# Performance work log

Measured on AMD Instinct MI355X. Metric: run time of the kernel, lower is better.

Reference implementation:

```python
import jax, jax.numpy as jnp
import numpy as np

EPS = 1e-5

def conv3x3(x, W, b):
    # NCHW 3x3 conv, padding=1 (SAME)
    y = jax.lax.conv_general_dilated(x, W, (1, 1), ((1, 1), (1, 1)),
                                     dimension_numbers=('NCHW', 'OIHW', 'NCHW'))
    return y + b[None, :, None, None]

def bn_relu(x, gamma, beta):
    # BatchNorm2d in training mode: batch statistics over (N,H,W)
    m = x.mean(axis=(0, 2, 3), keepdims=True)
    v = x.var(axis=(0, 2, 3), keepdims=True)
    xn = (x - m) * jax.lax.rsqrt(v + EPS)
    return jax.nn.relu(xn * gamma[None, :, None, None] + beta[None, :, None, None])

def haar_dwt2(x):
    # pywt.dwt2(x, 'db1') for even H,W: cA=LL, cH=row-detail/col-approx,
    # cV=row-approx/col-detail, cD=HH; each 0.5*(+-a +-b +-c +-d)
    a = x[:, :, 0::2, 0::2]
    b = x[:, :, 0::2, 1::2]
    c = x[:, :, 1::2, 0::2]
    d = x[:, :, 1::2, 1::2]
    cA = (a + b + c + d) * 0.5
    cH = (a + b - c - d) * 0.5
    cV = (a - b + c - d) * 0.5
    cD = (a - b - c + d) * 0.5
    return jnp.concatenate([cA, cH, cV, cD], axis=1)  # [B, 4C, H/2, W/2]

def setup_inputs() -> dict:
    key = jax.random.key(0)
    ks = jax.random.split(key, 4)
    B, Cin, Cout, H, W = 8, 64, 128, 256, 256
    inputs = jax.random.normal(ks[0], (B, Cin, H, W), dtype=jnp.float32)
    W1 = jax.random.normal(ks[1], (Cout, Cin, 3, 3), dtype=jnp.float32) * 0.05
    W2 = jax.random.normal(ks[2], (Cout, Cout, 3, 3), dtype=jnp.float32) * 0.05
    W3 = jax.random.normal(ks[3], (Cout, 4 * Cout, 3, 3), dtype=jnp.float32) * 0.05
    z = jnp.zeros((Cout,), jnp.float32)
    o = jnp.ones((Cout,), jnp.float32)
    return {"inputs": inputs,
            "W1": W1, "b1": z, "g1": o, "be1": z,
            "W2": W2, "b2": z, "g2": o, "be2": z,
            "W3": W3, "b3": z, "g3": o, "be3": z}

def reference(inputs, W1, b1, g1, be1, W2, b2, g2, be2, W3, b3, g3, be3):
    h = bn_relu(conv3x3(inputs, W1, b1), g1, be1)
    skip_con = bn_relu(conv3x3(h, W2, b2), g2, be2)          # [B, out_c, H, W]
    # original detaches before the pywt round-trip
    dwt = haar_dwt2(jax.lax.stop_gradient(skip_con))          # [B, 4*out_c, H/2, W/2]
    dwt_out = bn_relu(conv3x3(dwt, W3, b3), g3, be3)          # [B, out_c, H/2, W/2]
    return (skip_con, dwt_out)
```

## Files before the change

### kernel.cpp

```cpp
#include <hip/hip_runtime.h>

typedef __attribute__((ext_vector_type(8))) short bf16x8;
typedef __attribute__((ext_vector_type(4))) short bf16x4;
typedef __attribute__((ext_vector_type(4))) float f32x4;

__device__ __forceinline__ float bf2f(ushort u) {
  union { unsigned int i; float f; } v; v.i = ((unsigned int)u) << 16; return v.f;
}
__device__ __forceinline__ ushort f2bf(float f) {
  union { float f; unsigned int i; } v; v.f = f;
  unsigned int x = v.i;
  unsigned int r = (x + 0x7fffu + ((x >> 16) & 1u)) >> 16;
  return (ushort)r;
}

__device__ __forceinline__ void gload_lds16(const ushort* g, ushort* l) {
  __builtin_amdgcn_global_load_lds((const __attribute__((address_space(1))) void*)g,
                                   (__attribute__((address_space(3))) void*)l, 16, 0, 0);
}

__global__ void zero_f32(float* p, int n) {
  int i = blockIdx.x * 256 + threadIdx.x;
  if (i < n) p[i] = 0.f;
}

__global__ void pack_w(const float* __restrict__ W, ushort* __restrict__ Wp, int Cin) {
  int ncic = Cin >> 5;
  int total = 9 * ncic * 8 * 64 * 8;
  for (int idx = blockIdx.x * 256 + threadIdx.x; idx < total; idx += gridDim.x * 256) {
    int j = idx & 7;
    int l = (idx >> 3) & 63;
    int cf = (idx >> 9) & 7;
    int rest = idx >> 12;
    int cic = rest % ncic;
    int tap = rest / ncic;
    int co = cf * 16 + (l & 15);
    int ci = cic * 32 + ((l >> 4) * 8) + j;
    int ky = tap / 3, kx = tap % 3;
    Wp[idx] = f2bf(W[((co * Cin + ci) * 3 + ky) * 3 + kx]);
  }
}

__global__ __launch_bounds__(256)
void nchw2nhwc(const float* __restrict__ in, ushort* __restrict__ out) {
  const int n  = blockIdx.y;
  const int p0 = blockIdx.x << 6;
  const int tid = threadIdx.x;
  __shared__ ushort t[64 * 72];
  {
    int c  = tid >> 2;
    int pq = (tid & 3) << 4;
    const float* ip = in + (((size_t)(n * 64 + c)) << 16) + p0 + pq;
#pragma unroll
    for (int k = 0; k < 4; ++k) {
      float4 f = *(const float4*)(ip + k * 4);
      int p = pq + k * 4;
      t[(p + 0) * 72 + c] = f2bf(f.x);
      t[(p + 1) * 72 + c] = f2bf(f.y);
      t[(p + 2) * 72 + c] = f2bf(f.z);
      t[(p + 3) * 72 + c] = f2bf(f.w);
    }
  }
  __syncthreads();
#pragma unroll
  for (int k = 0; k < 2; ++k) {
    int id = k * 256 + tid;
    int cj = id & 7, p = id >> 3;
    bf16x8 v = *(const bf16x8*)&t[p * 72 + cj * 8];
    *(bf16x8*)(out + ((((size_t)n << 16) + p0 + p) << 6) + cj * 8) = v;
  }
}

__device__ __forceinline__ bf16x8 bnrelu8(bf16x8 v, const float* __restrict__ coef, int c0) {
  float4 a0 = *(const float4*)(coef + c0);
  float4 a1 = *(const float4*)(coef + c0 + 4);
  float4 b0 = *(const float4*)(coef + 128 + c0);
  float4 b1 = *(const float4*)(coef + 128 + c0 + 4);
  bf16x8 r;
  r[0] = (short)f2bf(fmaxf(a0.x * bf2f((ushort)v[0]) + b0.x, 0.f));
  r[1] = (short)f2bf(fmaxf(a0.y * bf2f((ushort)v[1]) + b0.y, 0.f));
  r[2] = (short)f2bf(fmaxf(a0.z * bf2f((ushort)v[2]) + b0.z, 0.f));
  r[3] = (short)f2bf(fmaxf(a0.w * bf2f((ushort)v[3]) + b0.w, 0.f));
  r[4] = (short)f2bf(fmaxf(a1.x * bf2f((ushort)v[4]) + b1.x, 0.f));
  r[5] = (short)f2bf(fmaxf(a1.y * bf2f((ushort)v[5]) + b1.y, 0.f));
  r[6] = (short)f2bf(fmaxf(a1.z * bf2f((ushort)v[6]) + b1.z, 0.f));
  r[7] = (short)f2bf(fmaxf(a1.w * bf2f((ushort)v[7]) + b1.w, 0.f));
  return r;
}

template<int MODE>
__global__ __launch_bounds__(256)
void conv_reg(const ushort* __restrict__ src, const ushort* __restrict__ Wp,
              const float* __restrict__ bias, const float* __restrict__ coef,
              ushort* __restrict__ out, float* __restrict__ sSum, float* __restrict__ sSsq,
              int Cin, int H, int W)
{
  const int ncic = Cin >> 5;
  const int x0 = blockIdx.x << 6;
  const int y0 = blockIdx.y << 1;
  const int n  = blockIdx.z;
  const int tid = threadIdx.x;
  const int wv = tid >> 6, l = tid & 63, l15 = l & 15, l4 = l >> 4;

  __shared__ __align__(16) char smem[17408];
  ushort* lds = (ushort*)smem;
  ushort* eps = (ushort*)smem;

  f32x4 acc[2][2][4];
#pragma unroll
  for (int yr = 0; yr < 2; ++yr)
#pragma unroll
    for (int f = 0; f < 2; ++f)
#pragma unroll
      for (int xf = 0; xf < 4; ++xf) acc[yr][f][xf] = (f32x4){0.f, 0.f, 0.f, 0.f};

  const size_t HW = (size_t)H * W;

  for (int cic = 0; cic < ncic; ++cic) {
    __syncthreads();
    for (int i = tid; i < 1056; i += 256) {
      int cj = i & 3;
      int t = i >> 2;
      int row = t / 66;
      int xt = t - row * 66;
      int ry = y0 + row - 1;
      int gx = x0 + xt - 1;
      bf16x8 v = {};
      if ((unsigned)ry < (unsigned)H && (unsigned)gx < (unsigned)W) {
        const ushort* p = src + ((size_t)n * HW + (size_t)ry * W + gx) * Cin + (cic << 5) + (cj << 3);
        v = *(const bf16x8*)p;
        if (MODE == 1) v = bnrelu8(v, coef, (cic << 5) + (cj << 3));
      }
      *(bf16x8*)&lds[(((row << 2) | cj) * 66 + xt) << 3] = v;
    }
    __syncthreads();

#pragma unroll
    for (int tap = 0; tap < 9; ++tap) {
      const int ky = tap / 3, kx = tap % 3;
      bf16x8 afr[2];
#pragma unroll
      for (int f = 0; f < 2; ++f) {
        const int cf = (wv << 1) | f;
        afr[f] = *(const bf16x8*)(Wp + (((size_t)(tap * ncic + cic) * 8 + cf) * 64 + l) * 8);
      }
      bf16x8 bfr[2][4];
#pragma unroll
      for (int yr = 0; yr < 2; ++yr)
#pragma unroll
        for (int xf = 0; xf < 4; ++xf) {
          int row = yr + ky;
          int xt = (xf << 4) + l15 + kx;
          bfr[yr][xf] = *(const bf16x8*)&lds[(((row << 2) | l4) * 66 + xt) << 3];
        }
#pragma unroll
      for (int f = 0; f < 2; ++f)
#pragma unroll
        for (int yr = 0; yr < 2; ++yr)
#pragma unroll
          for (int xf = 0; xf < 4; ++xf)
            acc[yr][f][xf] = __builtin_amdgcn_mfma_f32_16x16x32_bf16(afr[f], bfr[yr][xf], acc[yr][f][xf], 0, 0, 0);
    }
  }

  float sm[2][4] = {{0.f}}, sq[2][4] = {{0.f}};
  const int cb = (wv << 5) + (l4 << 2);
  for (int yr = 0; yr < 2; ++yr) {
    __syncthreads();
#pragma unroll
    for (int f = 0; f < 2; ++f) {
      const int cf = cb + (f << 4);
      float4 bv = *(const float4*)(bias + cf);
#pragma unroll
      for (int xf = 0; xf < 4; ++xf) {
        float v0 = acc[yr][f][xf][0] + bv.x;
        float v1 = acc[yr][f][xf][1] + bv.y;
        float v2 = acc[yr][f][xf][2] + bv.z;
        float v3 = acc[yr][f][xf][3] + bv.w;
        sm[f][0] += v0; sq[f][0] += v0 * v0;
        sm[f][1] += v1; sq[f][1] += v1 * v1;
        sm[f][2] += v2; sq[f][2] += v2 * v2;
        sm[f][3] += v3; sq[f][3] += v3 * v3;
        bf16x4 u;
        u[0] = (short)f2bf(v0); u[1] = (short)f2bf(v1);
        u[2] = (short)f2bf(v2); u[3] = (short)f2bf(v3);
        *(bf16x4*)&eps[((xf << 4) + l15) * 136 + cf] = u;
      }
    }
    __syncthreads();
    {
      const int xx = tid >> 2, c0 = (tid & 3) << 5;
      ushort* op = out + ((size_t)n * HW + (size_t)(y0 + yr) * W + x0 + xx) * 128 + c0;
#pragma unroll
      for (int k = 0; k < 4; ++k)
        *(bf16x8*)(op + (k << 3)) = *(const bf16x8*)&eps[xx * 136 + c0 + (k << 3)];
    }
  }

  const int rep = (int)((blockIdx.z * gridDim.y + blockIdx.y) * gridDim.x + blockIdx.x) & 31;
#pragma unroll
  for (int f = 0; f < 2; ++f)
#pragma unroll
    for (int j = 0; j < 4; ++j) {
      float s = sm[f][j], q = sq[f][j];
#pragma unroll
      for (int o = 1; o < 16; o <<= 1) { s += __shfl_xor(s, o); q += __shfl_xor(q, o); }
      if (l15 == 0) {
        int co = cb + (f << 4) + j;
        atomicAdd(&sSum[rep * 128 + co], s);
        atomicAdd(&sSsq[rep * 128 + co], q);
      }
    }
}

__global__ __launch_bounds__(256)
void conv_dma(const ushort* __restrict__ src, const ushort* __restrict__ Wp,
              const float* __restrict__ bias,
              ushort* __restrict__ out, float* __restrict__ sSum, float* __restrict__ sSsq,
              int Cin, int H, int W)
{
  const int ncic = Cin >> 5;
  const int x0 = blockIdx.x << 6;
  const int y0 = blockIdx.y << 1;
  const int n  = blockIdx.z;
  const int tid = threadIdx.x;
  const int wv = tid >> 6, l = tid & 63, l15 = l & 15, l4 = l >> 4;

  __shared__ __align__(16) ushort smem[2 * 8448];

  const size_t HW = (size_t)H * W;
  const ushort* srcn = src + (size_t)n * HW * Cin;

  int off[5];
#pragma unroll
  for (int it = 0; it < 5; ++it) {
    int i = it * 256 + tid;
    int cj = i & 3, p = i >> 2;
    int row = p / 66, xt = p - row * 66;
    int ry = y0 + row - 1, gx = x0 + xt - 1;
    bool ok = (i < 1056) && ((unsigned)ry < (unsigned)H) && ((unsigned)gx < (unsigned)W);
    off[it] = ok ? (int)((ry * W + gx) * Cin + (cj << 3)) : -1;
  }

  if (x0 == 0 || x0 + 64 >= W || y0 == 0 || y0 + 2 >= H) {
    for (int k = tid; k < 2112; k += 256) *(bf16x8*)&smem[k << 3] = (bf16x8){};
  }
  __syncthreads();

  f32x4 acc[2][2][4];
#pragma unroll
  for (int yr = 0; yr < 2; ++yr)
#pragma unroll
    for (int f = 0; f < 2; ++f)
#pragma unroll
      for (int xf = 0; xf < 4; ++xf) acc[yr][f][xf] = (f32x4){0.f, 0.f, 0.f, 0.f};

  auto STAGE = [&](ushort* buf, int cic) {
    const int coff = cic << 5;
#pragma unroll
    for (int it = 0; it < 5; ++it) {
      ushort* ldst = buf + ((it < 4 ? (it * 256 + (wv << 6)) : 1024) << 3);
      if (off[it] >= 0)
        gload_lds16(srcn + off[it] + coff, ldst);
    }
  };

  auto COMPUTE = [&](const ushort* buf, int cic) {
#pragma unroll
    for (int tap = 0; tap < 9; ++tap) {
      const int ky = tap / 3, kx = tap % 3;
      bf16x8 afr[2];
#pragma unroll
      for (int f = 0; f < 2; ++f) {
        const int cf = (wv << 1) | f;
        afr[f] = *(const bf16x8*)(Wp + (((size_t)(tap * ncic + cic) * 8 + cf) * 64 + l) * 8);
      }
      bf16x8 bfr[2][4];
#pragma unroll
      for (int yr = 0; yr < 2; ++yr)
#pragma unroll
        for (int xf = 0; xf < 4; ++xf) {
          int row = yr + ky;
          int xt = (xf << 4) + l15 + kx;
          bfr[yr][xf] = *(const bf16x8*)&buf[((((row * 66 + xt) << 2) | l4)) << 3];
        }
#pragma unroll
      for (int f = 0; f < 2; ++f)
#pragma unroll
        for (int yr = 0; yr < 2; ++yr)
#pragma unroll
          for (int xf = 0; xf < 4; ++xf)
            acc[yr][f][xf] = __builtin_amdgcn_mfma_f32_16x16x32_bf16(afr[f], bfr[yr][xf], acc[yr][f][xf], 0, 0, 0);
    }
  };

  STAGE(smem, 0);
  __syncthreads();

  int cur = 0;
  for (int cic = 0; cic < ncic; ++cic) {
    if (cic + 1 < ncic) STAGE(smem + (cur ^ 1) * 8448, cic + 1);
    COMPUTE(smem + cur * 8448, cic);
    __syncthreads();
    cur ^= 1;
  }

  float sm[2][4] = {{0.f}}, sq[2][4] = {{0.f}};
  ushort* eps = smem;
  const int cb = (wv << 5) + (l4 << 2);
  for (int yr = 0; yr < 2; ++yr) {
    __syncthreads();
#pragma unroll
    for (int f = 0; f < 2; ++f) {
      const int cf = cb + (f << 4);
      float4 bv = *(const float4*)(bias + cf);
#pragma unroll
      for (int xf = 0; xf < 4; ++xf) {
        float v0 = acc[yr][f][xf][0] + bv.x;
        float v1 = acc[yr][f][xf][1] + bv.y;
        float v2 = acc[yr][f][xf][2] + bv.z;
        float v3 = acc[yr][f][xf][3] + bv.w;
        sm[f][0] += v0; sq[f][0] += v0 * v0;
        sm[f][1] += v1; sq[f][1] += v1 * v1;
        sm[f][2] += v2; sq[f][2] += v2 * v2;
        sm[f][3] += v3; sq[f][3] += v3 * v3;
        bf16x4 u;
        u[0] = (short)f2bf(v0); u[1] = (short)f2bf(v1);
        u[2] = (short)f2bf(v2); u[3] = (short)f2bf(v3);
        *(bf16x4*)&eps[((xf << 4) + l15) * 136 + cf] = u;
      }
    }
    __syncthreads();
    {
      const int xx = tid >> 2, c0 = (tid & 3) << 5;
      ushort* op = out + ((size_t)n * HW + (size_t)(y0 + yr) * W + x0 + xx) * 128 + c0;
#pragma unroll
      for (int k = 0; k < 4; ++k)
        *(bf16x8*)(op + (k << 3)) = *(const bf16x8*)&eps[xx * 136 + c0 + (k << 3)];
    }
  }

  const int rep = (int)((blockIdx.z * gridDim.y + blockIdx.y) * gridDim.x + blockIdx.x) & 31;
#pragma unroll
  for (int f = 0; f < 2; ++f)
#pragma unroll
    for (int j = 0; j < 4; ++j) {
      float s = sm[f][j], q = sq[f][j];
#pragma unroll
      for (int o = 1; o < 16; o <<= 1) { s += __shfl_xor(s, o); q += __shfl_xor(q, o); }
      if (l15 == 0) {
        int co = cb + (f << 4) + j;
        atomicAdd(&sSum[rep * 128 + co], s);
        atomicAdd(&sSsq[rep * 128 + co], q);
      }
    }
}

__global__ void bn_finalize(const float* __restrict__ sSum, const float* __restrict__ sSsq,
                            const float* __restrict__ g, const float* __restrict__ be,
                            float* __restrict__ coef, float invN)
{
  int c = threadIdx.x;
  float S = 0.f, Q = 0.f;
  for (int r = 0; r < 32; ++r) { S += sSum[r * 128 + c]; Q += sSsq[r * 128 + c]; }
  float m = S * invN;
  float v = Q * invN - m * m;
  float a = g[c] / sqrtf(v + 1e-5f);
  coef[c] = a;
  coef[128 + c] = be[c] - m * a;
}

__global__ __launch_bounds__(256)
void skip_dwt2(const ushort* __restrict__ skipRaw, const float* __restrict__ coef,
               float* __restrict__ outSkip, ushort* __restrict__ dwt)
{
  const int x0 = blockIdx.x << 6;
  const int oy = blockIdx.y;
  const int n  = blockIdx.z >> 2;
  const int ct = blockIdx.z & 3;
  const int y0 = oy << 1;
  const int tid = threadIdx.x;
  __shared__ float t32[32 * 2 * 68];

#pragma unroll
  for (int it = 0; it < 2; ++it) {
    int i = it * 256 + tid;
    int cj = i & 3, x = (i >> 2) & 63, r = i >> 8;
    int c0 = (ct << 5) + (cj << 3);
    bf16x8 v = *(const bf16x8*)(skipRaw + (((size_t)n << 16) + (size_t)(y0 + r) * 256 + x0 + x) * 128 + c0);
    float4 a0 = *(const float4*)(coef + c0);
    float4 a1 = *(const float4*)(coef + c0 + 4);
    float4 b0 = *(const float4*)(coef + 128 + c0);
    float4 b1 = *(const float4*)(coef + 128 + c0 + 4);
    float av[8] = {a0.x, a0.y, a0.z, a0.w, a1.x, a1.y, a1.z, a1.w};
    float bv[8] = {b0.x, b0.y, b0.z, b0.w, b1.x, b1.y, b1.z, b1.w};
    int cl = cj << 3;
#pragma unroll
    for (int k = 0; k < 8; ++k)
      t32[((cl + k) * 2 + r) * 68 + x] = fmaxf(av[k] * bf2f((ushort)v[k]) + bv[k], 0.f);
  }
  __syncthreads();

  {
    int c = tid >> 3, x8 = (tid & 7) << 3;
    float* op = outSkip + (((size_t)(n * 128 + (ct << 5) + c)) << 16) + (size_t)y0 * 256 + x0 + x8;
#pragma unroll
    for (int r = 0; r < 2; ++r) {
      float4 r0 = *(const float4*)&t32[(c * 2 + r) * 68 + x8];
      float4 r1 = *(const float4*)&t32[(c * 2 + r) * 68 + x8 + 4];
      *(float4*)(op + (size_t)r * 256) = r0;
      *(float4*)(op + (size_t)r * 256 + 4) = r1;
    }
  }

  if (tid < 128) {
    int cj = tid & 3, ox = tid >> 2;
    int cl = cj << 3;
    bf16x8 oA, oH, oV, oD;
#pragma unroll
    for (int k = 0; k < 8; ++k) {
      int c = cl + k;
      float p00 = t32[(c * 2 + 0) * 68 + 2 * ox];
      float p01 = t32[(c * 2 + 0) * 68 + 2 * ox + 1];
      float p10 = t32[(c * 2 + 1) * 68 + 2 * ox];
      float p11 = t32[(c * 2 + 1) * 68 + 2 * ox + 1];
      oA[k] = (short)f2bf((p00 + p01 + p10 + p11) * 0.5f);
      oH[k] = (short)f2bf((p00 + p01 - p10 - p11) * 0.5f);
      oV[k] = (short)f2bf((p00 - p01 + p10 - p11) * 0.5f);
      oD[k] = (short)f2bf((p00 - p01 - p10 + p11) * 0.5f);
    }
    size_t db = ((size_t)n * 16384 + (size_t)oy * 128 + (x0 >> 1) + ox) * 512 + (ct << 5) + cl;
    *(bf16x8*)(dwt + db)       = oA;
    *(bf16x8*)(dwt + db + 128) = oH;
    *(bf16x8*)(dwt + db + 256) = oV;
    *(bf16x8*)(dwt + db + 384) = oD;
  }
}

__global__ __launch_bounds__(256)
void bn_transpose_out(const ushort* __restrict__ src, const float* __restrict__ coef,
                      float* __restrict__ dst, int H, int W)
{
  const int n  = blockIdx.z >> 2;
  const int cc = blockIdx.z & 3;
  const int x0 = blockIdx.x << 6;
  const int y  = blockIdx.y;
  const int tid = threadIdx.x;
  __shared__ float t[32 * 68];
  const size_t HW = (size_t)H * W;
  {
    int p = tid >> 2, cj = tid & 3;
    int c0 = (cc << 5) + (cj << 3);
    bf16x8 v = *(const bf16x8*)(src + ((size_t)n * HW + (size_t)y * W + x0 + p) * 128 + c0);
    float4 a0 = *(const float4*)(coef + c0);
    float4 a1 = *(const float4*)(coef + c0 + 4);
    float4 b0 = *(const float4*)(coef + 128 + c0);
    float4 b1 = *(const float4*)(coef + 128 + c0 + 4);
    int cl = cj << 3;
    t[(cl + 0) * 68 + p] = fmaxf(a0.x * bf2f((ushort)v[0]) + b0.x, 0.f);
    t[(cl + 1) * 68 + p] = fmaxf(a0.y * bf2f((ushort)v[1]) + b0.y, 0.f);
    t[(cl + 2) * 68 + p] = fmaxf(a0.z * bf2f((ushort)v[2]) + b0.z, 0.f);
    t[(cl + 3) * 68 + p] = fmaxf(a0.w * bf2f((ushort)v[3]) + b0.w, 0.f);
    t[(cl + 4) * 68 + p] = fmaxf(a1.x * bf2f((ushort)v[4]) + b1.x, 0.f);
    t[(cl + 5) * 68 + p] = fmaxf(a1.y * bf2f((ushort)v[5]) + b1.y, 0.f);
    t[(cl + 6) * 68 + p] = fmaxf(a1.z * bf2f((ushort)v[6]) + b1.z, 0.f);
    t[(cl + 7) * 68 + p] = fmaxf(a1.w * bf2f((ushort)v[7]) + b1.w, 0.f);
  }
  __syncthreads();
  {
    int c = tid >> 3, x8 = (tid & 7) << 3;
    float4 r0 = *(const float4*)&t[c * 68 + x8];
    float4 r1 = *(const float4*)&t[c * 68 + x8 + 4];
    float* op = dst + ((size_t)(n * 128 + (cc << 5) + c)) * HW + (size_t)y * W + x0 + x8;
    *(float4*)op = r0;
    *(float4*)(op + 4) = r1;
  }
}

extern "C" void kernel_launch(void* const* d_in, const int* in_sizes, int n_in,
                              void* d_out, int out_size, void* d_ws, size_t ws_size,
                              hipStream_t stream)
{
  const float* input = (const float*)d_in[0];
  const float* W1  = (const float*)d_in[1];
  const float* b1  = (const float*)d_in[2];
  const float* g1  = (const float*)d_in[3];
  const float* be1 = (const float*)d_in[4];
  const float* W2  = (const float*)d_in[5];
  const float* b2  = (const float*)d_in[6];
  const float* g2  = (const float*)d_in[7];
  const float* be2 = (const float*)d_in[8];
  const float* W3  = (const float*)d_in[9];
  const float* b3  = (const float*)d_in[10];
  const float* g3  = (const float*)d_in[11];
  const float* be3 = (const float*)d_in[12];

  char* ws = (char*)d_ws;
  ushort* h_raw    = (ushort*)(ws + 0);
  ushort* skip_raw = (ushort*)(ws + 134217728);
  ushort* dwt      = (ushort*)(ws + 268435456);
  ushort* in_nhwc  = (ushort*)(ws + 268435456);
  ushort* raw3     = (ushort*)(ws + 402653184);
  float*  stats    = (float*)(ws + 436207616);
  float*  s1 = stats,          *q1 = stats + 4096;
  float*  s2 = stats + 8192,   *q2 = stats + 12288;
  float*  s3 = stats + 16384,  *q3 = stats + 20480;
  float*  coef = (float*)(ws + 436305920);
  float*  c1 = coef, *c2 = coef + 256, *c3 = coef + 512;
  ushort* Wp1 = (ushort*)(ws + 436308992);
  ushort* Wp2 = (ushort*)(ws + 436456448);
  ushort* Wp3 = (ushort*)(ws + 436751360);

  zero_f32<<<96, 256, 0, stream>>>(stats, 24576);
  pack_w<<<288, 256, 0, stream>>>(W1, Wp1, 64);
  pack_w<<<576, 256, 0, stream>>>(W2, Wp2, 128);
  pack_w<<<2304, 256, 0, stream>>>(W3, Wp3, 512);
  nchw2nhwc<<<dim3(1024, 8), 256, 0, stream>>>(input, in_nhwc);

  conv_dma<<<dim3(4, 128, 8), 256, 0, stream>>>(in_nhwc, Wp1, b1,
                                                h_raw, s1, q1, 64, 256, 256);
  bn_finalize<<<1, 128, 0, stream>>>(s1, q1, g1, be1, c1, 1.f / 524288.f);

  conv_reg<1><<<dim3(4, 128, 8), 256, 0, stream>>>(h_raw, Wp2, b2, c1,
                                                   skip_raw, s2, q2, 128, 256, 256);
  bn_finalize<<<1, 128, 0, stream>>>(s2, q2, g2, be2, c2, 1.f / 524288.f);

  skip_dwt2<<<dim3(4, 128, 32), 256, 0, stream>>>(skip_raw, c2, (float*)d_out, dwt);

  conv_dma<<<dim3(2, 64, 8), 256, 0, stream>>>(dwt, Wp3, b3,
                                               raw3, s3, q3, 512, 128, 128);
  bn_finalize<<<1, 128, 0, stream>>>(s3, q3, g3, be3, c3, 1.f / 131072.f);

  bn_transpose_out<<<dim3(2, 128, 32), 256, 0, stream>>>(raw3, c3, (float*)d_out + 67108864, 128, 128);
}
```

Before: 696.3 us.

## Sweep conv down 16 rows with rolling 4-row LDS ring buffer

Replaces the per-2-row conv_reg kernel with conv_yp. Each block now walks 16 output rows and keeps a 4-row circular buffer of all input channels in LDS, so halo rows are loaded once instead of being reloaded by neighbouring blocks. It is also used for conv1 in place of conv_dma. The grid shrinks 8x, which costs parallelism and adds serial stage/compute phases with no overlap between the loads and the MFMA work. The LDS footprint grows to about 72KB, which lowers occupancy.

Measured after the change: 755.8 us. +8.6%, slower.

```diff
diff --git a/kernel.cpp b/kernel.cpp
--- a/kernel.cpp
+++ b/kernel.cpp
@@ -88,116 +88,135 @@
   return r;
 }
 
-template<int MODE>
+template<int MODE, int NCIC>
 __global__ __launch_bounds__(256)
-void conv_reg(const ushort* __restrict__ src, const ushort* __restrict__ Wp,
-              const float* __restrict__ bias, const float* __restrict__ coef,
-              ushort* __restrict__ out, float* __restrict__ sSum, float* __restrict__ sSsq,
-              int Cin, int H, int W)
+void conv_yp(const ushort* __restrict__ src, const ushort* __restrict__ Wp,
+             const float* __restrict__ bias, const float* __restrict__ coef,
+             ushort* __restrict__ out, float* __restrict__ sSum, float* __restrict__ sSsq,
+             int H, int W)
 {
-  const int ncic = Cin >> 5;
+  constexpr int Cin = NCIC * 32;
+  constexpr int CIP = 136;
+  constexpr int PLANE = 66 * CIP;
   const int x0 = blockIdx.x << 6;
-  const int y0 = blockIdx.y << 1;
+  const int ysBase = blockIdx.y << 4;
   const int n  = blockIdx.z;
   const int tid = threadIdx.x;
   const int wv = tid >> 6, l = tid & 63, l15 = l & 15, l4 = l >> 4;
 
-  __shared__ __align__(16) char smem[17408];
-  ushort* lds = (ushort*)smem;
-  ushort* eps = (ushort*)smem;
-
-  f32x4 acc[2][2][4];
-#pragma unroll
-  for (int yr = 0; yr < 2; ++yr)
-#pragma unroll
-    for (int f = 0; f < 2; ++f)
-#pragma unroll
-      for (int xf = 0; xf < 4; ++xf) acc[yr][f][xf] = (f32x4){0.f, 0.f, 0.f, 0.f};
+  __shared__ __align__(16) ushort smem[4 * PLANE];
 
   const size_t HW = (size_t)H * W;
-
-  for (int cic = 0; cic < ncic; ++cic) {
-    __syncthreads();
-    for (int i = tid; i < 1056; i += 256) {
-      int cj = i & 3;
-      int t = i >> 2;
-      int row = t / 66;
-      int xt = t - row * 66;
-      int ry = y0 + row - 1;
+  const ushort* srcn = src + (size_t)n * HW * Cin;
+
+  auto STAGE2 = [&](int r0) {
+    constexpr int NCJ = NCIC * 4;
+    constexpr int NCH = 2 * 66 * NCJ;
+    for (int i = tid; i < NCH; i += 256) {
+      int cj = i & (NCJ - 1);
+      int t  = i / NCJ;
+      int xt = t % 66;
+      int r  = t / 66;
+      int ry = r0 + r;
       int gx = x0 + xt - 1;
       bf16x8 v = {};
       if ((unsigned)ry < (unsigned)H && (unsigned)gx < (unsigned)W) {
-        const ushort* p = src + ((size_t)n * HW + (size_t)ry * W + gx) * Cin + (cic << 5) + (cj << 3);
-        v = *(const bf16x8*)p;
-        if (MODE == 1) v = bnrelu8(v, coef, (cic << 5) + (cj << 3));
-      }
-      *(bf16x8*)&lds[(((row << 2) | cj) * 66 + xt) << 3] = v;
-    }
-    __syncthreads();
-
-#pragma unroll
-    for (int tap = 0; tap < 9; ++tap) {
-      const int ky = tap / 3, kx = tap % 3;
-      bf16x8 afr[2];
-#pragma unroll
-      for (int f = 0; f < 2; ++f) {
-        const int cf = (wv << 1) | f;
-        afr[f] = *(const bf16x8*)(Wp + (((size_t)(tap * ncic + cic) * 8 + cf) * 64 + l) * 8);
-      }
-      bf16x8 bfr[2][4];
-#pragma unroll
-      for (int yr = 0; yr < 2; ++yr)
-#pragma unroll
-        for (int xf = 0; xf < 4; ++xf) {
-          int row = yr + ky;
-          int xt = (xf << 4) + l15 + kx;
-          bfr[yr][xf] = *(const bf16x8*)&lds[(((row << 2) | l4) * 66 + xt) << 3];
-        }
-#pragma unroll
-      for (int f = 0; f < 2; ++f)
-#pragma unroll
-        for (int yr = 0; yr < 2; ++yr)
-#pragma unroll
-          for (int xf = 0; xf < 4; ++xf)
-            acc[yr][f][xf] = __builtin_amdgcn_mfma_f32_16x16x32_bf16(afr[f], bfr[yr][xf], acc[yr][f][xf], 0, 0, 0);
-    }
-  }
+        v = *(const bf16x8*)(srcn + ((size_t)ry * W + gx) * Cin + (cj << 3));
+        if (MODE == 1) v = bnrelu8(v, coef, cj << 3);
+      }
+      *(bf16x8*)&smem[(ry & 3) * PLANE + xt * CIP + (cj << 3)] = v;
+    }
+  };
+
+  STAGE2(ysBase - 1);
+  STAGE2(ysBase + 1);
+  __syncthreads();
 
   float sm[2][4] = {{0.f}}, sq[2][4] = {{0.f}};
   const int cb = (wv << 5) + (l4 << 2);
-  for (int yr = 0; yr < 2; ++yr) {
+  const int rep = (int)((blockIdx.z * gridDim.y + blockIdx.y) * gridDim.x + blockIdx.x) & 31;
+
+  for (int step = 0; step < 8; ++step) {
+    const int ys = ysBase + (step << 1);
+
+    f32x4 acc[2][2][4];
+#pragma unroll
+    for (int yr = 0; yr < 2; ++yr)
+#pragma unroll
+      for (int f = 0; f < 2; ++f)
+#pragma unroll
+        for (int xf = 0; xf < 4; ++xf) acc[yr][f][xf] = (f32x4){0.f, 0.f, 0.f, 0.f};
+
+    for (int cic = 0; cic < NCIC; ++cic) {
+#pragma unroll
+      for (int tap = 0; tap < 9; ++tap) {
+        const int ky = tap / 3, kx = tap % 3;
+        bf16x8 afr[2];
+#pragma unroll
+        for (int f = 0; f < 2; ++f) {
+          const int cf = (wv << 1) | f;
+          afr[f] = *(const bf16x8*)(Wp + (((size_t)(tap * NCIC + cic) * 8 + cf) * 64 + l) * 8);
+        }
+        bf16x8 bfr[2][4];
+#pragma unroll
+        for (int yr = 0; yr < 2; ++yr)
+#pragma unroll
+          for (int xf = 0; xf < 4; ++xf) {
+            int aRow = ys + yr - 1 + ky;
+            bfr[yr][xf] = *(const bf16x8*)&smem[(aRow & 3) * PLANE +
+                                               ((xf << 4) + l15 + kx) * CIP +
+                                               (cic << 5) + (l4 << 3)];
+          }
+#pragma unroll
+        for (int f = 0; f < 2; ++f)
+#pragma unroll
+          for (int yr = 0; yr < 2; ++yr)
+#pragma unroll
+            for (int xf = 0; xf < 4; ++xf)
+              acc[yr][f][xf] = __builtin_amdgcn_mfma_f32_16x16x32_bf16(afr[f], bfr[yr][xf], acc[yr][f][xf], 0, 0, 0);
+      }
+    }
+
     __syncthreads();
-#pragma unroll
-    for (int f = 0; f < 2; ++f) {
-      const int cf = cb + (f << 4);
-      float4 bv = *(const float4*)(bias + cf);
-#pragma unroll
-      for (int xf = 0; xf < 4; ++xf) {
-        float v0 = acc[yr][f][xf][0] + bv.x;
-        float v1 = acc[yr][f][xf][1] + bv.y;
-        float v2 = acc[yr][f][xf][2] + bv.z;
-        float v3 = acc[yr][f][xf][3] + bv.w;
-        sm[f][0] += v0; sq[f][0] += v0 * v0;
-        sm[f][1] += v1; sq[f][1] += v1 * v1;
-        sm[f][2] += v2; sq[f][2] += v2 * v2;
-        sm[f][3] += v3; sq[f][3] += v3 * v3;
-        bf16x4 u;
-        u[0] = (short)f2bf(v0); u[1] = (short)f2bf(v1);
-        u[2] = (short)f2bf(v2); u[3] = (short)f2bf(v3);
-        *(bf16x4*)&eps[((xf << 4) + l15) * 136 + cf] = u;
+    ushort* eps = &smem[((ys - 1) & 3) * PLANE];
+    for (int yr = 0; yr < 2; ++yr) {
+      if (yr) __syncthreads();
+#pragma unroll
+      for (int f = 0; f < 2; ++f) {
+        const int cf = cb + (f << 4);
+        float4 bv = *(const float4*)(bias + cf);
+#pragma unroll
+        for (int xf = 0; xf < 4; ++xf) {
+          float v0 = acc[yr][f][xf][0] + bv.x;
+          float v1 = acc[yr][f][xf][1] + bv.y;
+          float v2 = acc[yr][f][xf][2] + bv.z;
+          float v3 = acc[yr][f][xf][3] + bv.w;
+          sm[f][0] += v0; sq[f][0] += v0 * v0;
+          sm[f][1] += v1; sq[f][1] += v1 * v1;
+          sm[f][2] += v2; sq[f][2] += v2 * v2;
+          sm[f][3] += v3; sq[f][3] += v3 * v3;
+          bf16x4 u;
+          u[0] = (short)f2bf(v0); u[1] = (short)f2bf(v1);
+          u[2] = (short)f2bf(v2); u[3] = (short)f2bf(v3);
+          *(bf16x4*)&eps[((xf << 4) + l15) * 136 + cf] = u;
+        }
+      }
+      __syncthreads();
+      {
+        const int xx = tid >> 2, c0 = (tid & 3) << 5;
+        ushort* op = out + ((size_t)n * HW + (size_t)(ys + yr) * W + x0 + xx) * 128 + c0;
+#pragma unroll
+        for (int k = 0; k < 4; ++k)
+          *(bf16x8*)(op + (k << 3)) = *(const bf16x8*)&eps[xx * 136 + c0 + (k << 3)];
       }
     }
     __syncthreads();
-    {
-      const int xx = tid >> 2, c0 = (tid & 3) << 5;
-      ushort* op = out + ((size_t)n * HW + (size_t)(y0 + yr) * W + x0 + xx) * 128 + c0;
-#pragma unroll
-      for (int k = 0; k < 4; ++k)
-        *(bf16x8*)(op + (k << 3)) = *(const bf16x8*)&eps[xx * 136 + c0 + (k << 3)];
-    }
-  }
-
-  const int rep = (int)((blockIdx.z * gridDim.y + blockIdx.y) * gridDim.x + blockIdx.x) & 31;
+    if (step < 7) {
+      STAGE2(ys + 3);
+      __syncthreads();
+    }
+  }
+
 #pragma unroll
   for (int f = 0; f < 2; ++f)
 #pragma unroll
@@ -517,12 +536,12 @@
   pack_w<<<2304, 256, 0, stream>>>(W3, Wp3, 512);
   nchw2nhwc<<<dim3(1024, 8), 256, 0, stream>>>(input, in_nhwc);
 
-  conv_dma<<<dim3(4, 128, 8), 256, 0, stream>>>(in_nhwc, Wp1, b1,
-                                                h_raw, s1, q1, 64, 256, 256);
+  conv_yp<0, 2><<<dim3(4, 16, 8), 256, 0, stream>>>(in_nhwc, Wp1, b1, nullptr,
+                                                    h_raw, s1, q1, 256, 256);
   bn_finalize<<<1, 128, 0, stream>>>(s1, q1, g1, be1, c1, 1.f / 524288.f);
 
-  conv_reg<1><<<dim3(4, 128, 8), 256, 0, stream>>>(h_raw, Wp2, b2, c1,
-                                                   skip_raw, s2, q2, 128, 256, 256);
+  conv_yp<1, 4><<<dim3(4, 16, 8), 256, 0, stream>>>(h_raw, Wp2, b2, c1,
+                                                    skip_raw, s2, q2, 256, 256);
   bn_finalize<<<1, 128, 0, stream>>>(s2, q2, g2, be2, c2, 1.f / 524288.f);
 
   skip_dwt2<<<dim3(4, 128, 32), 256, 0, stream>>>(skip_raw, c2, (float*)d_out, dwt);
```
